# Optimization experiments

Hardware: AMD Instinct MI355X
Metric: run time of the kernel (lower is better)

Reference implementation:

```python
import jax, jax.numpy as jnp
import numpy as np

jax.config.update("jax_enable_x64", True)  # hash uses int64 multiply-xor like torch .long()

NUM_LEVELS = 16
LEVEL_DIM = 2
PER_LEVEL_SCALE = 2
BASE_RES = 16
LOG2_HASHMAP = 19
PS1 = 19349663  # second spatial hash prime (ps[0] == 1)
N_POINTS = 524288


def _isprime(n):
    for p in range(2, int(n ** 0.5) + 1):
        if n % p == 0:
            return False
    return True


N_ENTRIES = 2 ** LOG2_HASHMAP
while not _isprime(N_ENTRIES):
    N_ENTRIES += 1  # -> 524309

SCALES = []
OFFSETS = [0]
START_HASH = NUM_LEVELS  # module uses -1 sentinel; NUM_LEVELS == 'no hashing yet'
for i in range(NUM_LEVELS):
    res = int(BASE_RES * PER_LEVEL_SCALE ** i)
    SCALES.append(res)
    n = (res + 1) ** 2
    if n > N_ENTRIES:
        if START_HASH == NUM_LEVELS:
            START_HASH = i
        n = N_ENTRIES
    OFFSETS.append(OFFSETS[-1] + n)
TABLE_SIZE = OFFSETS[-1]  # 5594552

CORNERS = jnp.array([[0.0, 0.0], [0.0, 1.0], [1.0, 0.0], [1.0, 1.0]], dtype=jnp.float32)  # [4,2]
SCALES_F = jnp.array(SCALES, dtype=jnp.float32)          # [L]
SCALES_I = jnp.array(SCALES, dtype=jnp.int64)            # [L]
LEVEL_OFF = jnp.array(OFFSETS[:-1], dtype=jnp.int64)     # [L] base offset per level


def setup_inputs() -> dict:
    key = jax.random.key(0)
    k1, k2 = jax.random.split(key)
    x = jax.random.uniform(k1, (N_POINTS, 2), dtype=jnp.float32)  # coords in [0,1)
    data = (jax.random.uniform(k2, (TABLE_SIZE, LEVEL_DIM), dtype=jnp.float32) * 2.0 - 1.0) * 1e-4
    return {"x": x, "data": data}


def reference(x, data):
    L, F = NUM_LEVELS, LEVEL_DIM
    float_x = x[None] * SCALES_F[:, None, None]                                  # [L,N,2]
    int_x = (float_x[:, :, None, :] + CORNERS[None, None]).astype(jnp.int64)     # [L,N,4,2]
    offset_x = float_x - int_x[:, :, 0].astype(float_x.dtype)                    # [L,N,2] frac part
    ix0, ix1 = int_x[..., 0], int_x[..., 1]
    # dense-grid index for low levels, spatial hash for high levels
    grid_ind = ix0 * (SCALES_I + 1)[:, None, None] + ix1                         # [L,N,4]
    hash_ind = (ix0 ^ (ix1 * PS1)) % N_ENTRIES                                   # [L,N,4]
    is_grid = (jnp.arange(L) < START_HASH)[:, None, None]
    ind = jnp.where(is_grid, grid_ind, hash_ind) + LEVEL_OFF[:, None, None]      # [L,N,4]
    val = data[ind]                                                              # [L,N,4,F]
    # bilinear corner weights: clamp(1 - c + (2c-1)*frac) per axis, product over xy
    w = jnp.clip(1.0 - CORNERS[None, None] + (2.0 * CORNERS[None, None] - 1.0) * offset_x[:, :, None], 0.0, 1.0)
    w = w[..., 0] * w[..., 1]                                                    # [L,N,4]
    out = jnp.einsum('lnc,lncf->lnf', w, val)                                    # [L,N,F]
    return out.transpose(1, 0, 2).reshape(-1, L * F)                             # [N, L*F]
```

## Files before the change

### kernel.cpp

```cpp
#include <hip/hip_runtime.h>


static constexpr int  kPoints    = 524288;
static constexpr int  kLevels    = 16;
static constexpr int  kStartHash = 6;
static constexpr unsigned kPs1     = 19349663u;
static constexpr unsigned kEntries = 524309u;
static constexpr unsigned kR32     = 352277u;

typedef float v2f __attribute__((ext_vector_type(2)));
typedef float v4f __attribute__((ext_vector_type(4)));

__device__ __forceinline__ void nt_store2(float2* p, const float2 v) {
    v2f t; t.x = v.x; t.y = v.y;
    __builtin_nontemporal_store(t, (v2f*)p);
}
__device__ __forceinline__ float2 nt_load2(const float2* p) {
    const v2f t = __builtin_nontemporal_load((const v2f*)p);
    return make_float2(t.x, t.y);
}
__device__ __forceinline__ void nt_store4(float4* p, const float4 v) {
    v4f t; t.x = v.x; t.y = v.y; t.z = v.z; t.w = v.w;
    __builtin_nontemporal_store(t, (v4f*)p);
}

__constant__ unsigned c_level_off[kLevels] = {
    0u, 289u, 1378u, 5603u, 22244u, 88293u, 351462u,
    875771u, 1400080u, 1924389u, 2448698u, 2973007u,
    3497316u, 4021625u, 4545934u, 5070243u
};

struct Corners {
    float    w00, w01, w10, w11;
    unsigned i00, i01, i10, i11;
};

__device__ __forceinline__ Corners prep_level(const float2 p, const int l)
{
    const int   scale_i = 16 << l;
    const float scale_f = (float)scale_i;

    const float fx = p.x * scale_f;
    const float fy = p.y * scale_f;

    const unsigned ix0 = (unsigned)(int)fx;
    const unsigned iy0 = (unsigned)(int)fy;
    const unsigned ix1 = (unsigned)(int)(fx + 1.0f);
    const unsigned iy1 = (unsigned)(int)(fy + 1.0f);

    const float ox = fx - (float)ix0;
    const float oy = fy - (float)iy0;

    const float wx1 = fminf(fmaxf(ox, 0.0f), 1.0f);
    const float wx0 = fminf(fmaxf(1.0f - ox, 0.0f), 1.0f);
    const float wy1 = fminf(fmaxf(oy, 0.0f), 1.0f);
    const float wy0 = fminf(fmaxf(1.0f - oy, 0.0f), 1.0f);

    unsigned i00, i01, i10, i11;
    if (l < kStartHash) {
        const unsigned stride = (unsigned)(scale_i + 1);
        i00 = ix0 * stride + iy0;
        i01 = ix0 * stride + iy1;
        i10 = ix1 * stride + iy0;
        i11 = ix1 * stride + iy1;
    } else {
        const unsigned long long hy0 = (unsigned long long)iy0 * kPs1;
        const unsigned long long hy1 = (unsigned long long)iy1 * kPs1;
        const unsigned lo0 = (unsigned)hy0, hi0 = (unsigned)(hy0 >> 32);
        const unsigned lo1 = (unsigned)hy1, hi1 = (unsigned)(hy1 >> 32);
        const unsigned a0 = (hi0 * kR32) % kEntries;
        const unsigned a1 = (hi1 * kR32) % kEntries;
        i00 = a0 + ((lo0 ^ ix0) % kEntries); if (i00 >= kEntries) i00 -= kEntries;
        i01 = a1 + ((lo1 ^ ix0) % kEntries); if (i01 >= kEntries) i01 -= kEntries;
        i10 = a0 + ((lo0 ^ ix1) % kEntries); if (i10 >= kEntries) i10 -= kEntries;
        i11 = a1 + ((lo1 ^ ix1) % kEntries); if (i11 >= kEntries) i11 -= kEntries;
    }

    Corners c;
    const unsigned base = c_level_off[l];
    c.i00 = base + i00; c.i01 = base + i01;
    c.i10 = base + i10; c.i11 = base + i11;
    c.w00 = wx0 * wy0;  c.w01 = wx0 * wy1;
    c.w10 = wx1 * wy0;  c.w11 = wx1 * wy1;
    return c;
}

__device__ __forceinline__ float2 finish_level(
    const Corners& c, const float2* __restrict__ tbl)
{
    const float2 v00 = tbl[c.i00];
    const float2 v01 = tbl[c.i01];
    const float2 v10 = tbl[c.i10];
    const float2 v11 = tbl[c.i11];
    return make_float2(
        c.w00 * v00.x + c.w01 * v01.x + c.w10 * v10.x + c.w11 * v11.x,
        c.w00 * v00.y + c.w01 * v01.y + c.w10 * v10.y + c.w11 * v11.y);
}

__global__ __launch_bounds__(256) void level_pass(
    const float2* __restrict__ x,
    const float2* __restrict__ tbl,
    float2* __restrict__ ws)
{
    const int b    = blockIdx.x;
    const int xcd  = b & 7;
    const int slot = b >> 3;

    int level, pblk;
    if (slot < 1024) {
        level = 6 + xcd;
        pblk  = slot;
    } else if (slot < 1152) {
        level = 14;
        pblk  = xcd * 128 + (slot - 1024);
    } else if (slot < 1280) {
        level = 15;
        pblk  = xcd * 128 + (slot - 1152);
    } else {
        const int d = xcd * 768 + (slot - 1280);
        level = d >> 10;
        pblk  = d & 1023;
    }

    const int n0 = (pblk << 9) | threadIdx.x;
    const int n1 = n0 + 256;
    const float2 pA = x[n0];
    const float2 pB = x[n1];

    const Corners cA = prep_level(pA, level);
    const Corners cB = prep_level(pB, level);

    const float2 a00 = tbl[cA.i00], a01 = tbl[cA.i01];
    const float2 a10 = tbl[cA.i10], a11 = tbl[cA.i11];
    const float2 b00 = tbl[cB.i00], b01 = tbl[cB.i01];
    const float2 b10 = tbl[cB.i10], b11 = tbl[cB.i11];

    const float2 rA = make_float2(
        cA.w00 * a00.x + cA.w01 * a01.x + cA.w10 * a10.x + cA.w11 * a11.x,
        cA.w00 * a00.y + cA.w01 * a01.y + cA.w10 * a10.y + cA.w11 * a11.y);
    const float2 rB = make_float2(
        cB.w00 * b00.x + cB.w01 * b01.x + cB.w10 * b10.x + cB.w11 * b11.x,
        cB.w00 * b00.y + cB.w01 * b01.y + cB.w10 * b10.y + cB.w11 * b11.y);

    const size_t tile0 = (size_t)(n0 >> 8);
    nt_store2(&ws[(tile0 << 12) + (level << 8) + (n0 & 255)], rA);
    nt_store2(&ws[((tile0 + 1) << 12) + (level << 8) + (n1 & 255)], rB);
}

static constexpr int kTStride = 257;

__global__ __launch_bounds__(256) void transpose_out(
    const float2* __restrict__ ws,
    float4* __restrict__ out)
{
    __shared__ float2 lds[kLevels * kTStride];

    const int t = threadIdx.x;
    const float2* __restrict__ tile = ws + ((size_t)blockIdx.x << 12);

#pragma unroll
    for (int l = 0; l < kLevels; ++l)
        lds[l * kTStride + t] = nt_load2(&tile[(l << 8) + t]);

    __syncthreads();

    float4* o = out + ((size_t)blockIdx.x << 11);
#pragma unroll
    for (int k = 0; k < 8; ++k) {
        const int f  = k * 256 + t;
        const int nl = f >> 3;
        const int i  = t & 7;
        const float2 a = lds[(2 * i)     * kTStride + nl];
        const float2 b = lds[(2 * i + 1) * kTStride + nl];
        nt_store4(&o[f], make_float4(a.x, a.y, b.x, b.y));
    }
}

__global__ __launch_bounds__(256) void hashgrid_fwd(
    const float2* __restrict__ x,
    const float2* __restrict__ tbl,
    float4* __restrict__ out)
{
    const int n = blockIdx.x * blockDim.x + threadIdx.x;
    if (n >= kPoints) return;
    const float2 p = x[n];
    float acc[2 * kLevels];
#pragma unroll
    for (int l = 0; l < kLevels; ++l) {
        const float2 r = finish_level(prep_level(p, l), tbl);
        acc[2 * l + 0] = r.x;
        acc[2 * l + 1] = r.y;
    }
    float4* o = out + (size_t)n * 8;
#pragma unroll
    for (int i = 0; i < 8; ++i)
        o[i] = make_float4(acc[4 * i + 0], acc[4 * i + 1],
                           acc[4 * i + 2], acc[4 * i + 3]);
}

extern "C" void kernel_launch(void* const* d_in, const int* in_sizes, int n_in,
                              void* d_out, int out_size, void* d_ws, size_t ws_size,
                              hipStream_t stream) {
    const float2* x   = (const float2*)d_in[0];
    const float2* tbl = (const float2*)d_in[1];

    const size_t ws_needed = (size_t)kLevels * kPoints * sizeof(float2);
    if (ws_size >= ws_needed) {
        float2* ws = (float2*)d_ws;
        level_pass<<<kLevels * (kPoints / 512), 256, 0, stream>>>(x, tbl, ws);
        transpose_out<<<kPoints / 256, 256, 0, stream>>>(ws, (float4*)d_out);
    } else {
        hashgrid_fwd<<<kPoints / 256, 256, 0, stream>>>(x, tbl, (float4*)d_out);
    }
}
```

Before: 237.4 us.

## Fuse per-level gather and LDS transpose into a single kernel

Replaces the two-kernel scheme (per-level gather into a workspace, then a transpose pass) with one kernel where each thread computes all 16 levels for its point and writes them through LDS for coalesced output stores. This removes the workspace round trip through memory and one launch. In exchange it drops the XCD-aware level-to-block mapping, which kept each level's hash table slice local to one L2, so table gathers may get worse cache locality, and per-thread register pressure rises.

```diff
diff --git a/kernel.cpp b/kernel.cpp
--- a/kernel.cpp
+++ b/kernel.cpp
@@ -8,17 +8,8 @@
 static constexpr unsigned kEntries = 524309u;
 static constexpr unsigned kR32     = 352277u;
 
-typedef float v2f __attribute__((ext_vector_type(2)));
 typedef float v4f __attribute__((ext_vector_type(4)));
 
-__device__ __forceinline__ void nt_store2(float2* p, const float2 v) {
-    v2f t; t.x = v.x; t.y = v.y;
-    __builtin_nontemporal_store(t, (v2f*)p);
-}
-__device__ __forceinline__ float2 nt_load2(const float2* p) {
-    const v2f t = __builtin_nontemporal_load((const v2f*)p);
-    return make_float2(t.x, t.y);
-}
 __device__ __forceinline__ void nt_store4(float4* p, const float4 v) {
     v4f t; t.x = v.x; t.y = v.y; t.z = v.z; t.w = v.w;
     __builtin_nontemporal_store(t, (v4f*)p);
@@ -97,70 +88,27 @@
         c.w00 * v00.y + c.w01 * v01.y + c.w10 * v10.y + c.w11 * v11.y);
 }
 
-__global__ __launch_bounds__(256) void level_pass(
+static constexpr int kTStride = 257;
+
+__global__ __launch_bounds__(256) void fused_pass(
     const float2* __restrict__ x,
     const float2* __restrict__ tbl,
-    float2* __restrict__ ws)
-{
-    const int b    = blockIdx.x;
-    const int xcd  = b & 7;
-    const int slot = b >> 3;
-
-    int level, pblk;
-    if (slot < 1024) {
-        level = 6 + xcd;
-        pblk  = slot;
-    } else if (slot < 1152) {
-        level = 14;
-        pblk  = xcd * 128 + (slot - 1024);
-    } else if (slot < 1280) {
-        level = 15;
-        pblk  = xcd * 128 + (slot - 1152);
-    } else {
-        const int d = xcd * 768 + (slot - 1280);
-        level = d >> 10;
-        pblk  = d & 1023;
-    }
-
-    const int n0 = (pblk << 9) | threadIdx.x;
-    const int n1 = n0 + 256;
-    const float2 pA = x[n0];
-    const float2 pB = x[n1];
-
-    const Corners cA = prep_level(pA, level);
-    const Corners cB = prep_level(pB, level);
-
-    const float2 a00 = tbl[cA.i00], a01 = tbl[cA.i01];
-    const float2 a10 = tbl[cA.i10], a11 = tbl[cA.i11];
-    const float2 b00 = tbl[cB.i00], b01 = tbl[cB.i01];
-    const float2 b10 = tbl[cB.i10], b11 = tbl[cB.i11];
-
-    const float2 rA = make_float2(
-        cA.w00 * a00.x + cA.w01 * a01.x + cA.w10 * a10.x + cA.w11 * a11.x,
-        cA.w00 * a00.y + cA.w01 * a01.y + cA.w10 * a10.y + cA.w11 * a11.y);
-    const float2 rB = make_float2(
-        cB.w00 * b00.x + cB.w01 * b01.x + cB.w10 * b10.x + cB.w11 * b11.x,
-        cB.w00 * b00.y + cB.w01 * b01.y + cB.w10 * b10.y + cB.w11 * b11.y);
-
-    const size_t tile0 = (size_t)(n0 >> 8);
-    nt_store2(&ws[(tile0 << 12) + (level << 8) + (n0 & 255)], rA);
-    nt_store2(&ws[((tile0 + 1) << 12) + (level << 8) + (n1 & 255)], rB);
-}
-
-static constexpr int kTStride = 257;
-
-__global__ __launch_bounds__(256) void transpose_out(
-    const float2* __restrict__ ws,
     float4* __restrict__ out)
 {
     __shared__ float2 lds[kLevels * kTStride];
 
     const int t = threadIdx.x;
-    const float2* __restrict__ tile = ws + ((size_t)blockIdx.x << 12);
+    const int n = (blockIdx.x << 8) | t;
+    const float2 p = x[n];
+
+    float2 r[kLevels];
+#pragma unroll
+    for (int l = 0; l < kLevels; ++l)
+        r[l] = finish_level(prep_level(p, l), tbl);
 
 #pragma unroll
     for (int l = 0; l < kLevels; ++l)
-        lds[l * kTStride + t] = nt_load2(&tile[(l << 8) + t]);
+        lds[l * kTStride + t] = r[l];
 
     __syncthreads();
 
@@ -176,40 +124,10 @@
     }
 }
 
-__global__ __launch_bounds__(256) void hashgrid_fwd(
-    const float2* __restrict__ x,
-    const float2* __restrict__ tbl,
-    float4* __restrict__ out)
-{
-    const int n = blockIdx.x * blockDim.x + threadIdx.x;
-    if (n >= kPoints) return;
-    const float2 p = x[n];
-    float acc[2 * kLevels];
-#pragma unroll
-    for (int l = 0; l < kLevels; ++l) {
-        const float2 r = finish_level(prep_level(p, l), tbl);
-        acc[2 * l + 0] = r.x;
-        acc[2 * l + 1] = r.y;
-    }
-    float4* o = out + (size_t)n * 8;
-#pragma unroll
-    for (int i = 0; i < 8; ++i)
-        o[i] = make_float4(acc[4 * i + 0], acc[4 * i + 1],
-                           acc[4 * i + 2], acc[4 * i + 3]);
-}
-
 extern "C" void kernel_launch(void* const* d_in, const int* in_sizes, int n_in,
                               void* d_out, int out_size, void* d_ws, size_t ws_size,
                               hipStream_t stream) {
     const float2* x   = (const float2*)d_in[0];
     const float2* tbl = (const float2*)d_in[1];
-
-    const size_t ws_needed = (size_t)kLevels * kPoints * sizeof(float2);
-    if (ws_size >= ws_needed) {
-        float2* ws = (float2*)d_ws;
-        level_pass<<<kLevels * (kPoints / 512), 256, 0, stream>>>(x, tbl, ws);
-        transpose_out<<<kPoints / 256, 256, 0, stream>>>(ws, (float4*)d_out);
-    } else {
-        hashgrid_fwd<<<kPoints / 256, 256, 0, stream>>>(x, tbl, (float4*)d_out);
-    }
+    fused_pass<<<kPoints / 256, 256, 0, stream>>>(x, tbl, (float4*)d_out);
 }
```

Measured after the change: 286.9 us. 1.21x slower.
